# Optimization experiments

Measured on AMD Instinct MI355X. Metric: run time of the kernel, lower is better.

Reference implementation:

```python
import jax, jax.numpy as jnp
import numpy as np
from jax import lax

B, N, C = 32, 1024, 768
H_RES, W_RES = 32, 32
NUM_HEADS = 8
CH = C // NUM_HEADS  # 96
SCALE = CH ** -0.5


def setup_inputs() -> dict:
    key = jax.random.key(0)
    k1, k2, k3 = jax.random.split(key, 3)
    x = jax.random.normal(k1, (B, N, C), dtype=jnp.float32)
    # trunc_normal_(std=0.02) approximated by normal * 0.02
    w_qkv = jax.random.normal(k2, (3 * C, C), dtype=jnp.float32) * 0.02
    # conv init: normal(0, sqrt(2/fan_out)), fan_out = 3*3*C/groups = 9
    w_crpe = jax.random.normal(k3, (C, 1, 3, 3), dtype=jnp.float32) * np.sqrt(2.0 / 9.0)
    b_crpe = jnp.zeros((C,), dtype=jnp.float32)
    return {"x": x, "w_qkv": w_qkv, "w_crpe": w_crpe, "b_crpe": b_crpe}


def _forward(x, w_qkv, w_crpe, b_crpe):
    b, n, c = x.shape
    h, ch = NUM_HEADS, CH
    # qkv projection: [B,N,3C] -> [3,B,h,N,Ch]
    qkv = jnp.einsum('bnc,dc->bnd', x, w_qkv)
    qkv = qkv.reshape(b, n, 3, h, ch).transpose(2, 0, 3, 1, 4)
    q, k, v = qkv[0], qkv[1], qkv[2]  # each [B,h,N,Ch]
    # softmax over token dim (dim=2 of [B,h,N,Ch])
    k_softmax = jax.nn.softmax(k, axis=2)
    # dd_trans = k_softmax^T @ v : [B,h,Ch,Ch]
    dd_trans = jnp.einsum('bhnc,bhnd->bhcd', k_softmax, v)
    factor_attn = jnp.einsum('bhnc,bhcd->bhnd', q, dd_trans)  # [B,h,N,Ch]
    # crpe: depthwise 3x3 conv on v reshaped to image layout
    v_img = v.transpose(0, 1, 3, 2).reshape(b, c, H_RES, W_RES)  # B (h Ch) H W
    conv_v = lax.conv_general_dilated(
        v_img, w_crpe, window_strides=(1, 1), padding='SAME',
        feature_group_count=c,
        dimension_numbers=('NCHW', 'OIHW', 'NCHW'))
    conv_v = conv_v + b_crpe[None, :, None, None]
    conv_v = conv_v.reshape(b, h, ch, n).transpose(0, 1, 3, 2)  # [B,h,N,Ch]
    crpe = q * conv_v
    out = SCALE * factor_attn + crpe  # [B,h,N,Ch]
    return out.transpose(0, 2, 1, 3).reshape(b, n, c)


def reference(x, w_qkv, w_crpe, b_crpe):
    return _forward(x, w_qkv, w_crpe, b_crpe)
```

## Files before the change

kernel.cpp:

```cpp
#include <hip/hip_runtime.h>
#include <stdint.h>

#define B_SZ   32
#define N_TOK  1024
#define C_DIM  768
#define HEADS  8
#define CH_DIM 96
#define GM     32768
#define GN     2304
#define GK     768
#define SCALE_F 0.10206207261596577f
#define WHICH_STRIDE 25165824u
#define BH_STRIDE    98304u

typedef __attribute__((ext_vector_type(8))) short short8;
typedef __attribute__((ext_vector_type(8))) unsigned short ushort8;
typedef __attribute__((ext_vector_type(4))) float f32x4;
typedef __attribute__((ext_vector_type(4))) int int4v;

__device__ __forceinline__ float bf2f(unsigned short u) {
  union { unsigned int i; float f; } x; x.i = ((unsigned int)u) << 16; return x.f;
}
__device__ __forceinline__ unsigned short f2bf(float f) {
  union { float f; unsigned int i; } x; x.f = f;
  unsigned int r = x.i + 0x7fffu + ((x.i >> 16) & 1u);
  return (unsigned short)(r >> 16);
}

__device__ __forceinline__ void gload_lds16(const void* g, void* l) {
  __builtin_amdgcn_global_load_lds(
      (const __attribute__((address_space(1))) unsigned int*)g,
      (__attribute__((address_space(3))) unsigned int*)l, 16, 0, 0);
}

__global__ __launch_bounds__(256) void quant_rows(
    const float* __restrict__ x, const float* __restrict__ wq,
    signed char* __restrict__ xq, signed char* __restrict__ wqo,
    float* __restrict__ inv_x, float* __restrict__ inv_w) {
  const int row = blockIdx.x * 4 + (threadIdx.x >> 6);
  const int l = threadIdx.x & 63;
  const float* src; signed char* dst; float* inv; int r;
  if (row < GM) { src = x;  dst = xq;  inv = inv_x; r = row; }
  else { r = row - GM; if (r >= GN) return; src = wq; dst = wqo; inv = inv_w; }

  const float4* s4 = (const float4*)(src + (size_t)r * 768);
  float4 v0 = s4[l], v1 = s4[l + 64], v2 = s4[l + 128];
  float m = fmaxf(fmaxf(fmaxf(fabsf(v0.x), fabsf(v0.y)), fmaxf(fabsf(v0.z), fabsf(v0.w))),
                  fmaxf(fmaxf(fabsf(v1.x), fabsf(v1.y)), fmaxf(fabsf(v1.z), fabsf(v1.w))));
  m = fmaxf(m, fmaxf(fmaxf(fabsf(v2.x), fabsf(v2.y)), fmaxf(fabsf(v2.z), fabsf(v2.w))));
#pragma unroll
  for (int off = 32; off; off >>= 1) m = fmaxf(m, __shfl_xor(m, off));
  const float sc = 127.0f / m;
  if (l == 0) inv[r] = m * (1.0f / 127.0f);

  char4* d4 = (char4*)(dst + (size_t)r * 768);
  char4 o;
  o.x = (signed char)(int)rintf(v0.x * sc); o.y = (signed char)(int)rintf(v0.y * sc);
  o.z = (signed char)(int)rintf(v0.z * sc); o.w = (signed char)(int)rintf(v0.w * sc);
  d4[l] = o;
  o.x = (signed char)(int)rintf(v1.x * sc); o.y = (signed char)(int)rintf(v1.y * sc);
  o.z = (signed char)(int)rintf(v1.z * sc); o.w = (signed char)(int)rintf(v1.w * sc);
  d4[l + 64] = o;
  o.x = (signed char)(int)rintf(v2.x * sc); o.y = (signed char)(int)rintf(v2.y * sc);
  o.z = (signed char)(int)rintf(v2.z * sc); o.w = (signed char)(int)rintf(v2.w * sc);
  d4[l + 128] = o;
}

__global__ __launch_bounds__(512, 2) void qkv_gemm_i8(
    const signed char* __restrict__ xb,
    const signed char* __restrict__ wb,
    const float* __restrict__ inv_x,
    const float* __restrict__ inv_w,
    unsigned short* __restrict__ qkv) {
  __shared__ __align__(16) char lds[4][2][16384];

  const int t = threadIdx.x, w = t >> 6, l = t & 63;
  const int l15 = l & 15, lhi = l >> 4;

  const int bid = blockIdx.x;
  const int swz = (bid & 7) * 144 + (bid >> 3);
  const int brow = (swz / 9) * 256;
  const int bcol = (swz % 9) * 256;
  const int wr = w >> 2, wc = w & 3;

  const int s_colb = (((l & 3) ^ ((l >> 3) & 3)) << 4);
  const char* gA0 = (const char*)xb + (size_t)brow * 768 + s_colb;
  const char* gB0 = (const char*)wb + (size_t)bcol * 768 + s_colb;

  const int rd_sw = (lhi * 16) ^ (((l15 >> 1) & 3) << 4);
  const int a_off = (wr * 128 + l15) * 64 + rd_sw;
  const int b_off = (wc * 64 + l15) * 64 + rd_sw;

  int4v acc[8][4];
#pragma unroll
  for (int m = 0; m < 8; ++m)
#pragma unroll
    for (int n = 0; n < 4; ++n) acc[m][n] = (int4v){0, 0, 0, 0};

  auto STAGE = [&](int bi, int kt) {
#pragma unroll
    for (int rr = 0; rr < 2; ++rr) {
      const int rowA = (w + rr * 8) * 16 + (l >> 2);
      gload_lds16(gA0 + (size_t)rowA * 768 + kt * 64,
                  &lds[bi][0][(w + rr * 8) * 1024]);
      gload_lds16(gB0 + (size_t)rowA * 768 + kt * 64,
                  &lds[bi][1][(w + rr * 8) * 1024]);
    }
  };

  auto COMPUTE = [&](int bi) {
    int4v af[8], bf8[4];
#pragma unroll
    for (int n = 0; n < 4; ++n)
      bf8[n] = *(const int4v*)(&lds[bi][1][b_off + n * 1024]);
#pragma unroll
    for (int m = 0; m < 8; ++m)
      af[m] = *(const int4v*)(&lds[bi][0][a_off + m * 1024]);
    __builtin_amdgcn_s_setprio(1);
#pragma unroll
    for (int m = 0; m < 8; ++m)
#pragma unroll
      for (int n = 0; n < 4; ++n)
        acc[m][n] = __builtin_amdgcn_mfma_i32_16x16x64_i8(af[m], bf8[n], acc[m][n], 0, 0, 0);
    __builtin_amdgcn_s_setprio(0);
  };

#define BARSYNC_VM(n) do {                                  \
    __builtin_amdgcn_sched_barrier(0);                      \
    asm volatile("s_waitcnt vmcnt(" #n ")" ::: "memory");   \
    __builtin_amdgcn_sched_barrier(0);                      \
    __builtin_amdgcn_s_barrier();                           \
    __builtin_amdgcn_sched_barrier(0);                      \
  } while (0)

  STAGE(0, 0); STAGE(1, 1); STAGE(2, 2);
  BARSYNC_VM(8);

  for (int kt = 0; kt < 9; ++kt) {
    STAGE((kt + 3) & 3, kt + 3);
    COMPUTE(kt & 3);
    BARSYNC_VM(8);
  }
  COMPUTE(1); BARSYNC_VM(4);
  COMPUTE(2); BARSYNC_VM(0);
  COMPUTE(3);

  const int bb = brow / 1024;
#pragma unroll
  for (int m = 0; m < 8; ++m) {
    const int row0 = brow + wr * 128 + m * 16 + lhi * 4;
    const int tok0 = row0 & 1023;
    float ix[4];
#pragma unroll
    for (int r = 0; r < 4; ++r) ix[r] = inv_x[row0 + r];
#pragma unroll
    for (int n = 0; n < 4; ++n) {
      const int col   = bcol + wc * 64 + n * 16 + l15;
      const float dq0 = inv_w[col];
      const int which = col / 768;
      const int hh    = (col % 768) / 96;
      const int ch    = col % 96;
      unsigned short* dst = qkv + (size_t)which * WHICH_STRIDE
                          + ((size_t)(bb * 8 + hh)) * BH_STRIDE + ch;
#pragma unroll
      for (int r = 0; r < 4; ++r) {
        float v = (float)acc[m][n][r] * dq0 * ix[r];
        if (which == 1) v = __expf(v);
        dst[(size_t)(tok0 + r) * 96] = f2bf(v);
      }
    }
  }
#undef BARSYNC_VM
}

__global__ __launch_bounds__(512, 2) void dd_fused(
    const unsigned short* __restrict__ qkv,
    unsigned short* __restrict__ ddT) {
  __shared__ __align__(16) char smem[124416];
  unsigned short* stg = (unsigned short*)smem;
  float* facc = (float*)smem;
  float* fsum = (float*)(smem + 122880);
  float* sinv = (float*)(smem + 123648);

  const int bh = blockIdx.x;
  const int t = threadIdx.x, w = t >> 6, l = t & 63;
  const int l15 = l & 15, lhi = l >> 4;

  unsigned short* myK = stg + w * 7680;
  unsigned short* myV = myK + 3840;
  const int n   = l >> 1;
  const int chh = l & 1;
  const unsigned short* kb = qkv + WHICH_STRIDE     + (size_t)bh * BH_STRIDE;
  const unsigned short* vb = qkv + 2 * WHICH_STRIDE + (size_t)bh * BH_STRIDE;

  f32x4 acc[6][6], accS[6];
#pragma unroll
  for (int mf = 0; mf < 6; ++mf) {
    accS[mf] = (f32x4){0.f, 0.f, 0.f, 0.f};
#pragma unroll
    for (int nf = 0; nf < 6; ++nf) acc[mf][nf] = (f32x4){0.f, 0.f, 0.f, 0.f};
  }
  short8 ones;
#pragma unroll
  for (int j = 0; j < 8; ++j) ones[j] = (short)0x3F80;

  for (int tt = 0; tt < 4; ++tt) {
    const int n0 = w * 128 + tt * 32;
    const size_t g = (size_t)(n0 + n) * 96 + chh * 48;
#pragma unroll
    for (int i = 0; i < 6; ++i) {
      ushort8 k8 = *(const ushort8*)(kb + g + i * 8);
      ushort8 v8 = *(const ushort8*)(vb + g + i * 8);
      const int c0 = chh * 48 + i * 8;
#pragma unroll
      for (int j = 0; j < 8; ++j) {
        myK[(c0 + j) * 40 + n] = k8[j];
        myV[(c0 + j) * 40 + n] = v8[j];
      }
    }
    short8 af[6], bf8[6];
#pragma unroll
    for (int mf = 0; mf < 6; ++mf)
      af[mf] = *(const short8*)((const char*)myK + (mf * 16 + l15) * 80 + lhi * 16);
#pragma unroll
    for (int nf = 0; nf < 6; ++nf)
      bf8[nf] = *(const short8*)((const char*)myV + (nf * 16 + l15) * 80 + lhi * 16);
#pragma unroll
    for (int mf = 0; mf < 6; ++mf) {
#pragma unroll
      for (int nf = 0; nf < 6; ++nf)
        acc[mf][nf] = __builtin_amdgcn_mfma_f32_16x16x32_bf16(af[mf], bf8[nf], acc[mf][nf], 0, 0, 0);
      accS[mf] = __builtin_amdgcn_mfma_f32_16x16x32_bf16(af[mf], ones, accS[mf], 0, 0, 0);
    }
  }

  __syncthreads();
  float* fr  = facc + (w >> 2) * 9600;
  float* fsr = fsum + (w >> 2) * 96;
  for (int ww = 0; ww < 4; ++ww) {
    if ((w & 3) == ww) {
#pragma unroll
      for (int mf = 0; mf < 6; ++mf) {
#pragma unroll
        for (int nf = 0; nf < 6; ++nf) {
          const int c = mf * 16 + lhi * 4, d = nf * 16 + l15;
#pragma unroll
          for (int r = 0; r < 4; ++r) {
            float* p = fr + (size_t)(c + r) * 100 + d;
            if (ww == 0) *p = acc[mf][nf][r]; else *p += acc[mf][nf][r];
          }
        }
        if (l15 == 0) {
          const int c = mf * 16 + lhi * 4;
#pragma unroll
          for (int r = 0; r < 4; ++r) {
            if (ww == 0) fsr[c + r] = accS[mf][r];
            else         fsr[c + r] += accS[mf][r];
          }
        }
      }
    }
    __syncthreads();
  }
  for (int i = t; i < 9600; i += 512) facc[i] += facc[9600 + i];
  if (t < 96) fsum[t] += fsum[96 + t];
  __syncthreads();
  if (t < 96) sinv[t] = 1.0f / fsum[t];
  __syncthreads();

  unsigned short* dst = ddT + (size_t)bh * 9216;
#pragma unroll
  for (int e = 0; e < 18; ++e) {
    const int idx = t * 18 + e;
    const int d = idx / 96, c = idx % 96;
    dst[idx] = f2bf(facc[(size_t)c * 100 + d] * sinv[c]);
  }
}

__global__ __launch_bounds__(256) void factor_conv_p(
    const unsigned short* __restrict__ qkv,
    const unsigned short* __restrict__ ddT,
    const float* __restrict__ wcr,
    const float* __restrict__ bcr,
    float* __restrict__ outb) {
  __shared__ __align__(16) unsigned short sQ[64 * 96];
  __shared__ __align__(16) unsigned short sD[96 * 96];
  __shared__ __align__(16) unsigned short sV[128 * 96];
  __shared__ float sW[96 * 9];
  __shared__ float sBias[96];
  const int half = blockIdx.x, h = blockIdx.y, b = blockIdx.z;
  const int t = threadIdx.x, wv = t >> 6, l = t & 63;
  const int l15 = l & 15, lhi = l >> 4;
  const int bh = b * 8 + h;

  const char* dg = (const char*)ddT + (size_t)bh * 18432;
#pragma unroll
  for (int it = 0; it < 4; ++it)
    gload_lds16(dg + (it * 256 + t) * 16, (char*)sD + it * 4096 + wv * 1024);
  if (wv < 2)
    gload_lds16(dg + (1024 + t) * 16, (char*)sD + 16384 + wv * 1024);
  for (int i = t; i < 960; i += 256) {
    if (i < 864) sW[i] = wcr[(size_t)(h * 96) * 9 + i];
    else         sBias[i - 864] = bcr[h * 96 + (i - 864)];
  }

  const char* qg = (const char*)(qkv + (size_t)bh * BH_STRIDE);
  const char* vg = (const char*)(qkv + 2 * WHICH_STRIDE + (size_t)bh * BH_STRIDE);
  const int wrow = (wv >> 1) * 32;
  const int wcol = (wv & 1) * 48;

  for (int it8 = 0; it8 < 8; ++it8) {
    const int nt = half * 8 + it8;
    const int n0 = nt * 64, y0 = nt * 2;

#pragma unroll
    for (int it = 0; it < 3; ++it)
      gload_lds16(qg + (size_t)n0 * 192 + (it * 256 + t) * 16,
                  (char*)sQ + it * 4096 + wv * 1024);
#pragma unroll
    for (int it = 0; it < 6; ++it) {
      const int f = it * 256 + t;
      const int row = f / 12, ch = f % 12;
      int tok = n0 - 32 + row;
      tok = tok < 0 ? 0 : (tok > 1023 ? 1023 : tok);
      gload_lds16(vg + (size_t)tok * 192 + ch * 16,
                  (char*)sV + it * 4096 + wv * 1024);
    }
    __syncthreads();

    f32x4 acc[2][3];
#pragma unroll
    for (int m = 0; m < 2; ++m)
#pragma unroll
      for (int nn = 0; nn < 3; ++nn) acc[m][nn] = (f32x4){0.f, 0.f, 0.f, 0.f};

#pragma unroll
    for (int ks = 0; ks < 3; ++ks) {
      short8 af[2], bf8[3];
#pragma unroll
      for (int m = 0; m < 2; ++m)
        af[m] = *(const short8*)((const char*)sQ + (wrow + m*16 + l15) * 192 + ks * 64 + lhi * 16);
#pragma unroll
      for (int nn = 0; nn < 3; ++nn)
        bf8[nn] = *(const short8*)((const char*)sD + (wcol + nn*16 + l15) * 192 + ks * 64 + lhi * 16);
#pragma unroll
      for (int m = 0; m < 2; ++m)
#pragma unroll
        for (int nn = 0; nn < 3; ++nn)
          acc[m][nn] = __builtin_amdgcn_mfma_f32_16x16x32_bf16(af[m], bf8[nn], acc[m][nn], 0, 0, 0);
    }

#pragma unroll
    for (int nn = 0; nn < 3; ++nn) {
      const int dc = wcol + nn * 16 + l15;
      float w9[9];
#pragma unroll
      for (int k = 0; k < 9; ++k) w9[k] = sW[dc * 9 + k];
      const float bv = sBias[dc];
#pragma unroll
      for (int m = 0; m < 2; ++m) {
        const int rl0 = wrow + m * 16 + lhi * 4;
        const int x = rl0 & 31, yl = rl0 >> 5;
        float cs[3][6];
#pragma unroll
        for (int dy = 0; dy < 3; ++dy) {
          const int gy = y0 + yl + dy - 1;
          const bool vy = (gy >= 0) && (gy < 32);
#pragma unroll
          for (int i = 0; i < 6; ++i) {
            const int xx = x - 1 + i;
            cs[dy][i] = (vy && xx >= 0 && xx < 32)
                ? bf2f(sV[((yl + dy) * 32 + xx) * 96 + dc]) : 0.f;
          }
        }
#pragma unroll
        for (int r = 0; r < 4; ++r) {
          float conv = bv;
#pragma unroll
          for (int dy = 0; dy < 3; ++dy)
#pragma unroll
            for (int dx = 0; dx < 3; ++dx)
              conv += w9[dy * 3 + dx] * cs[dy][r + dx];
          const int row = rl0 + r;
          const float qv = bf2f(sQ[row * 96 + dc]);
          outb[((size_t)(b * N_TOK + n0 + row)) * C_DIM + h * 96 + dc] =
              SCALE_F * acc[m][nn][r] + qv * conv;
        }
      }
    }
    __syncthreads();
  }
}

extern "C" void kernel_launch(void* const* d_in, const int* in_sizes, int n_in,
                              void* d_out, int out_size, void* d_ws, size_t ws_size,
                              hipStream_t stream) {
  const float* x      = (const float*)d_in[0];
  const float* w_qkv  = (const float*)d_in[1];
  const float* w_crpe = (const float*)d_in[2];
  const float* b_crpe = (const float*)d_in[3];
  float* out = (float*)d_out;

  char* ws = (char*)d_ws;
  signed char*    xq    = (signed char*)ws;
  signed char*    wq    = (signed char*)(ws + 25165824);
  float*          inv_x = (float*)(ws + 27000832);
  float*          inv_w = (float*)(ws + 27131904);
  unsigned short* qkv   = (unsigned short*)(ws + 53870592);
  unsigned short* ddT   = (unsigned short*)(ws + 204865536);

  quant_rows<<<dim3((GM + GN + 3) / 4), 256, 0, stream>>>(
      x, w_qkv, xq, wq, inv_x, inv_w);
  qkv_gemm_i8<<<dim3(1152), 512, 0, stream>>>(xq, wq, inv_x, inv_w, qkv);
  dd_fused<<<dim3(B_SZ * HEADS), 512, 0, stream>>>(qkv, ddT);
  factor_conv_p<<<dim3(2, HEADS, B_SZ), 256, 0, stream>>>(qkv, ddT, w_crpe, b_crpe, out);
}
```

Before: 224.7 us.

## Shrink int8 QKV GEMM tile to 128x256 with double-buffered LDS

Halves the GEMM block tile height from 256 to 128 rows, so the grid doubles to 2304 blocks and the per-thread accumulator drops to 4x4 fragments. LDS goes from a 4-stage to a 2-stage buffer of 24KB each, and launch bounds rise to 4 blocks per CU. The aim is more occupancy and less LDS and register pressure. In exchange, each block reuses the B tile across fewer rows and the shallower prefetch pipeline hides less memory latency.

New measurement: 216.1 us. 1.04x faster.

```diff
diff --git a/kernel.cpp b/kernel.cpp
--- a/kernel.cpp
+++ b/kernel.cpp
@@ -66,20 +66,20 @@
   d4[l + 128] = o;
 }
 
-__global__ __launch_bounds__(512, 2) void qkv_gemm_i8(
+__global__ __launch_bounds__(512, 4) void qkv_gemm_i8(
     const signed char* __restrict__ xb,
     const signed char* __restrict__ wb,
     const float* __restrict__ inv_x,
     const float* __restrict__ inv_w,
     unsigned short* __restrict__ qkv) {
-  __shared__ __align__(16) char lds[4][2][16384];
+  __shared__ __align__(16) char lds[2][24576];
 
   const int t = threadIdx.x, w = t >> 6, l = t & 63;
   const int l15 = l & 15, lhi = l >> 4;
 
   const int bid = blockIdx.x;
-  const int swz = (bid & 7) * 144 + (bid >> 3);
-  const int brow = (swz / 9) * 256;
+  const int swz = (bid & 7) * 288 + (bid >> 3);
+  const int brow = (swz / 9) * 128;
   const int bcol = (swz % 9) * 256;
   const int wr = w >> 2, wc = w & 3;
 
@@ -88,67 +88,62 @@
   const char* gB0 = (const char*)wb + (size_t)bcol * 768 + s_colb;
 
   const int rd_sw = (lhi * 16) ^ (((l15 >> 1) & 3) << 4);
-  const int a_off = (wr * 128 + l15) * 64 + rd_sw;
-  const int b_off = (wc * 64 + l15) * 64 + rd_sw;
-
-  int4v acc[8][4];
-#pragma unroll
-  for (int m = 0; m < 8; ++m)
+  const int a_off = (wr * 64 + l15) * 64 + rd_sw;
+  const int b_off = 8192 + (wc * 64 + l15) * 64 + rd_sw;
+
+  int4v acc[4][4];
+#pragma unroll
+  for (int m = 0; m < 4; ++m)
 #pragma unroll
     for (int n = 0; n < 4; ++n) acc[m][n] = (int4v){0, 0, 0, 0};
 
   auto STAGE = [&](int bi, int kt) {
-#pragma unroll
-    for (int rr = 0; rr < 2; ++rr) {
-      const int rowA = (w + rr * 8) * 16 + (l >> 2);
-      gload_lds16(gA0 + (size_t)rowA * 768 + kt * 64,
-                  &lds[bi][0][(w + rr * 8) * 1024]);
-      gload_lds16(gB0 + (size_t)rowA * 768 + kt * 64,
-                  &lds[bi][1][(w + rr * 8) * 1024]);
-    }
+    const int rowL = w * 16 + (l >> 2);
+    gload_lds16(gA0 + (size_t)rowL * 768 + kt * 64,         &lds[bi][w * 1024]);
+    gload_lds16(gB0 + (size_t)rowL * 768 + kt * 64,         &lds[bi][8192 + w * 1024]);
+    gload_lds16(gB0 + (size_t)(rowL + 128) * 768 + kt * 64, &lds[bi][8192 + (w + 8) * 1024]);
   };
 
   auto COMPUTE = [&](int bi) {
-    int4v af[8], bf8[4];
+    int4v af[4], bf8[4];
 #pragma unroll
     for (int n = 0; n < 4; ++n)
-      bf8[n] = *(const int4v*)(&lds[bi][1][b_off + n * 1024]);
-#pragma unroll
-    for (int m = 0; m < 8; ++m)
-      af[m] = *(const int4v*)(&lds[bi][0][a_off + m * 1024]);
+      bf8[n] = *(const int4v*)(&lds[bi][b_off + n * 1024]);
+#pragma unroll
+    for (int m = 0; m < 4; ++m)
+      af[m] = *(const int4v*)(&lds[bi][a_off + m * 1024]);
     __builtin_amdgcn_s_setprio(1);
 #pragma unroll
-    for (int m = 0; m < 8; ++m)
+    for (int m = 0; m < 4; ++m)
 #pragma unroll
       for (int n = 0; n < 4; ++n)
         acc[m][n] = __builtin_amdgcn_mfma_i32_16x16x64_i8(af[m], bf8[n], acc[m][n], 0, 0, 0);
     __builtin_amdgcn_s_setprio(0);
   };
 
-#define BARSYNC_VM(n) do {                                  \
-    __builtin_amdgcn_sched_barrier(0);                      \
-    asm volatile("s_waitcnt vmcnt(" #n ")" ::: "memory");   \
-    __builtin_amdgcn_sched_barrier(0);                      \
-    __builtin_amdgcn_s_barrier();                           \
-    __builtin_amdgcn_sched_barrier(0);                      \
-  } while (0)
-
-  STAGE(0, 0); STAGE(1, 1); STAGE(2, 2);
-  BARSYNC_VM(8);
-
-  for (int kt = 0; kt < 9; ++kt) {
-    STAGE((kt + 3) & 3, kt + 3);
-    COMPUTE(kt & 3);
-    BARSYNC_VM(8);
-  }
-  COMPUTE(1); BARSYNC_VM(4);
-  COMPUTE(2); BARSYNC_VM(0);
-  COMPUTE(3);
+#define SB __builtin_amdgcn_sched_barrier(0)
+#define BAR do { SB; __builtin_amdgcn_s_barrier(); SB; } while (0)
+
+  STAGE(0, 0); STAGE(1, 1);
+  SB; asm volatile("s_waitcnt vmcnt(3)" ::: "memory");
+  BAR;
+
+  for (int kt = 0; kt < 12; ++kt) {
+    COMPUTE(kt & 1);
+    BAR;
+    if (kt < 10) {
+      STAGE(kt & 1, kt + 2);
+      SB; asm volatile("s_waitcnt vmcnt(3)" ::: "memory");
+    } else if (kt == 10) {
+      SB; asm volatile("s_waitcnt vmcnt(0)" ::: "memory");
+    }
+    BAR;
+  }
 
   const int bb = brow / 1024;
 #pragma unroll
-  for (int m = 0; m < 8; ++m) {
-    const int row0 = brow + wr * 128 + m * 16 + lhi * 4;
+  for (int m = 0; m < 4; ++m) {
+    const int row0 = brow + wr * 64 + m * 16 + lhi * 4;
     const int tok0 = row0 & 1023;
     float ix[4];
 #pragma unroll
@@ -170,7 +165,8 @@
       }
     }
   }
-#undef BARSYNC_VM
+#undef BAR
+#undef SB
 }
 
 __global__ __launch_bounds__(512, 2) void dd_fused(
@@ -411,7 +407,7 @@
 
   quant_rows<<<dim3((GM + GN + 3) / 4), 256, 0, stream>>>(
       x, w_qkv, xq, wq, inv_x, inv_w);
-  qkv_gemm_i8<<<dim3(1152), 512, 0, stream>>>(xq, wq, inv_x, inv_w, qkv);
+  qkv_gemm_i8<<<dim3(2304), 512, 0, stream>>>(xq, wq, inv_x, inv_w, qkv);
   dd_fused<<<dim3(B_SZ * HEADS), 512, 0, stream>>>(qkv, ddT);
   factor_conv_p<<<dim3(2, HEADS, B_SZ), 256, 0, stream>>>(qkv, ddT, w_crpe, b_crpe, out);
 }
```
